# Kernel optimization log

Hardware: AMD Instinct MI355X
Metric: run time of the kernel (lower is better)

Reference implementation:

```python
import jax, jax.numpy as jnp
import numpy as np

B, N, D_H, D_K = 1024, 200, 512, 512
C_CLIP = 10.0  # tanh clipping constant C from out_attention default


def setup_inputs() -> dict:
    key = jax.random.key(0)
    k1, k2, k3, k4, k5 = jax.random.split(key, 5)
    d_c = 3 * D_H
    # xavier_uniform-ish scale (gain 1.414) approximated with scaled normals
    s_q = 1.414 * (2.0 / (d_c + D_K)) ** 0.5
    s_k = 1.414 * (2.0 / (D_H + D_K)) ** 0.5
    return {
        "n": N,
        "H": jax.random.normal(k1, (B, N, D_H), dtype=jnp.float32),
        "W_Q": jax.random.normal(k2, (d_c, D_K), dtype=jnp.float32) * s_q,
        "W_K": jax.random.normal(k3, (D_H, D_K), dtype=jnp.float32) * s_k,
        "v_1": jax.random.normal(k4, (D_H,), dtype=jnp.float32) * 0.1,
        "v_f": jax.random.normal(k5, (D_H,), dtype=jnp.float32) * 0.1,
    }


def reference(n, H, W_Q, W_K, v_1, v_f):
    Bsz, n_nodes, d_h = H.shape
    d_k = W_K.shape[1]
    inv_sqrt_dk = 1.0 / jnp.sqrt(jnp.asarray(d_k, H.dtype))

    H_bar = jnp.mean(H, axis=-2)  # (B, d_h)  == 1/n * sum over nodes
    K = H @ W_K                   # (B, n, d_k): W_K fixed across steps, hoist out of loop

    h_c0 = jnp.concatenate(
        [H_bar,
         jnp.broadcast_to(v_1, (Bsz, d_h)),
         jnp.broadcast_to(v_f, (Bsz, d_h))], axis=-1)  # (B, 3*d_h)

    keys = jax.random.split(jax.random.key(42), n)
    batch_ix = jnp.arange(Bsz)

    def step(carry, xs):
        h_c, H_pi_1 = carry           # (B, 3dh), (B, dh)
        i, k = xs
        Q = h_c @ W_Q                 # (B, d_k)
        U = jnp.einsum('bk,bnk->bn', Q, K) * inv_sqrt_dk  # (B, n)
        logits = C_CLIP * jnp.tanh(U)
        # multinomial(softmax(logits), 1) == categorical(logits)
        pi = jax.random.categorical(k, logits, axis=-1)   # (B,)
        H_pi = H[batch_ix, pi]        # (B, d_h) row gather
        H_pi_1 = jnp.where(i == 0, H_pi, H_pi_1)          # freeze first pick
        h_c_new = jnp.concatenate([H_bar, H_pi, H_pi_1], axis=-1)
        return (h_c_new, H_pi_1), pi

    init = (h_c0, jnp.zeros_like(H_bar))
    _, pis = jax.lax.scan(step, init, (jnp.arange(n), keys))  # pis: (n, B)
    # original duplicates step-0 sample: Pi = cat(Pi_0, Pi_0, Pi_1, ..., Pi_{n-1})
    Pi = jnp.concatenate([pis[:1], pis], axis=0).T  # (B, n+1)
    return Pi
```

## Files before the change

### kernel.cpp

```cpp
#include <hip/hip_runtime.h>
#include <math.h>

#define BSZ 1024
#define NNODE 200
#define DH 512
#define DK 512
#define NSTEP 200
#define G 2
#define TPB 512

typedef float f4 __attribute__((ext_vector_type(4)));

__device__ __forceinline__ unsigned rotl32(unsigned x, int r) {
  return (x << r) | (x >> (32 - r));
}

__device__ __forceinline__ void tf2x32(unsigned k0, unsigned k1,
                                       unsigned c0, unsigned c1,
                                       unsigned& o0, unsigned& o1) {
  unsigned ks2 = k0 ^ k1 ^ 0x1BD11BDAu;
  unsigned x0 = c0 + k0, x1 = c1 + k1;
#define TF_RND(r) { x0 += x1; x1 = rotl32(x1, (r)); x1 ^= x0; }
  TF_RND(13) TF_RND(15) TF_RND(26) TF_RND(6)
  x0 += k1;  x1 += ks2 + 1u;
  TF_RND(17) TF_RND(29) TF_RND(16) TF_RND(24)
  x0 += ks2; x1 += k0 + 2u;
  TF_RND(13) TF_RND(15) TF_RND(26) TF_RND(6)
  x0 += k0;  x1 += k1 + 3u;
  TF_RND(17) TF_RND(29) TF_RND(16) TF_RND(24)
  x0 += k1;  x1 += ks2 + 4u;
  TF_RND(13) TF_RND(15) TF_RND(26) TF_RND(6)
  x0 += ks2; x1 += k0 + 5u;
#undef TF_RND
  o0 = x0; o1 = x1;
}

__device__ __forceinline__ void step_key(int i, unsigned& k0, unsigned& k1) {
  tf2x32(0u, 42u, 0u, (unsigned)i, k0, k1);
}
__device__ __forceinline__ unsigned elem_bits(unsigned k0, unsigned k1, unsigned m) {
  unsigned o0, o1;
  tf2x32(k0, k1, 0u, m, o0, o1);
  return o0 ^ o1;
}

__device__ __forceinline__ float xla_tanh_f32(float x) {
  const float kMax = 7.90531110763549805f;
  float xc = fminf(fmaxf(x, -kMax), kMax);
  float x2 = xc * xc;
  float p = -2.76076847742355e-16f;
  p = __builtin_fmaf(x2, p, 2.00018790482477e-13f);
  p = __builtin_fmaf(x2, p, -8.60467152213735e-11f);
  p = __builtin_fmaf(x2, p, 5.12229709037114e-08f);
  p = __builtin_fmaf(x2, p, 1.48572235717979e-05f);
  p = __builtin_fmaf(x2, p, 6.37261928875436e-04f);
  p = __builtin_fmaf(x2, p, 4.89352455891786e-03f);
  float num = xc * p;
  float q = 1.19825839466702e-06f;
  q = __builtin_fmaf(x2, q, 1.18534705686654e-04f);
  q = __builtin_fmaf(x2, q, 2.26843463243900e-03f);
  q = __builtin_fmaf(x2, q, 4.89352518554385e-03f);
  float r = num / q;
  return (fabsf(x) < 0.0004f) ? x : r;
}

__device__ __forceinline__ float xla_log_f32(float x) {
#pragma clang fp contract(off)
  unsigned bits = __float_as_uint(x);
  int e = (int)((bits >> 23) & 0xffu) - 126;
  float m = __uint_as_float((bits & 0x007fffffu) | 0x3f000000u);
  bool c = m < 0.707106781186547524f;
  e = c ? (e - 1) : e;
  m = c ? (m + m) : m;
  m = m - 1.0f;
  float z = m * m;
  float y = 7.0376836292e-2f;
  y = y * m + (-1.1514610310e-1f);
  y = y * m + 1.1676998740e-1f;
  y = y * m + (-1.2420140846e-1f);
  y = y * m + 1.4249322787e-1f;
  y = y * m + (-1.6668057665e-1f);
  y = y * m + 2.0000714765e-1f;
  y = y * m + (-2.4999993993e-1f);
  y = y * m + 3.3333331174e-1f;
  y = y * m;
  y = y * z;
  float ef = (float)e;
  float t1 = ef * (-2.12194440e-4f);
  y = y + t1;
  float t2 = z * 0.5f;
  y = y - t2;
  float r = m + y;
  float t3 = ef * 0.693359375f;
  r = r + t3;
  return r;
}

template<bool NT>
__device__ __forceinline__ float u_dot(const f4* __restrict__ Kb4,
                                       const float* __restrict__ qrow) {
  float l[16];
#pragma unroll
  for (int j = 0; j < 16; j++) l[j] = 0.0f;
#pragma unroll 1
  for (int g = 0; g < 8; g++) {
    f4 kv[16];
#pragma unroll
    for (int m = 0; m < 16; m++) {
      const f4* p = &Kb4[(size_t)(g * 16 + m) * NNODE];
      kv[m] = NT ? __builtin_nontemporal_load(p) : *p;
    }
    {
#pragma clang fp contract(off)
#pragma unroll
      for (int m = 0; m < 16; m++) {
        const int r = (4 * m) & 15;
        float p0 = kv[m][0] * qrow[g * 64 + 4 * m + 0];
        l[r + 0] = l[r + 0] + p0;
        float p1 = kv[m][1] * qrow[g * 64 + 4 * m + 1];
        l[r + 1] = l[r + 1] + p1;
        float p2 = kv[m][2] * qrow[g * 64 + 4 * m + 2];
        l[r + 2] = l[r + 2] + p2;
        float p3 = kv[m][3] * qrow[g * 64 + 4 * m + 3];
        l[r + 3] = l[r + 3] + p3;
      }
    }
  }
  {
#pragma clang fp contract(off)
#pragma unroll
    for (int j = 0; j < 8; j++) l[j] = l[j] + l[j + 8];
#pragma unroll
    for (int j = 0; j < 4; j++) l[j] = l[j] + l[j + 4];
#pragma unroll
    for (int j = 0; j < 2; j++) l[j] = l[j] + l[j + 2];
    return l[0] + l[1];
  }
}


__global__ void k_hbar(const float* __restrict__ H, float* __restrict__ Hbar) {
#pragma clang fp contract(off)
  int idx = blockIdx.x * 256 + threadIdx.x;
  int b = idx >> 9, d = idx & 511;
  const float* p = H + (size_t)b * NNODE * DH + d;
  float s = 0.0f;
  for (int n = 0; n < NNODE; n++) s = s + p[(size_t)n * DH];
  Hbar[idx] = s / 200.0f;
}

__global__ __launch_bounds__(256) void k_K(const float* __restrict__ H,
                                           const float* __restrict__ WK,
                                           float* __restrict__ KT) {
  __shared__ float hr[8][DH];
  __shared__ float ts[DK * 9];
  int g = blockIdx.x;
  int b = g / 25;
  int r0 = (g % 25) * 8;
  int t = threadIdx.x;
  const float* Hb = H + (size_t)b * NNODE * DH + (size_t)r0 * DH;
  for (int e = t; e < 8 * DH; e += 256) hr[e >> 9][e & 511] = Hb[e];
  __syncthreads();
  int k0 = t, k1 = t + 256;
  float a[8][2];
#pragma unroll
  for (int r = 0; r < 8; r++) { a[r][0] = 0.0f; a[r][1] = 0.0f; }
  for (int d = 0; d < DH; d++) {
    float w0 = WK[(size_t)d * DK + k0], w1 = WK[(size_t)d * DK + k1];
#pragma unroll
    for (int r = 0; r < 8; r++) {
      a[r][0] = __builtin_fmaf(hr[r][d], w0, a[r][0]);
      a[r][1] = __builtin_fmaf(hr[r][d], w1, a[r][1]);
    }
  }
#pragma unroll
  for (int r = 0; r < 8; r++) {
    ts[k0 * 9 + r] = a[r][0];
    ts[k1 * 9 + r] = a[r][1];
  }
  __syncthreads();
  float* Ko = KT + (size_t)b * DK * NNODE;
  for (int i = t; i < (DK / 4) * 8; i += 256) {
    int c = i >> 3, r = i & 7;
    float4 v = make_float4(ts[(4 * c + 0) * 9 + r], ts[(4 * c + 1) * 9 + r],
                           ts[(4 * c + 2) * 9 + r], ts[(4 * c + 3) * 9 + r]);
    *(float4*)(Ko + ((size_t)c * NNODE + (r0 + r)) * 4) = v;
  }
}

__global__ __launch_bounds__(256) void k_acc512(const float* __restrict__ Hbar,
                                                const float* __restrict__ WQ,
                                                float* __restrict__ acc) {
  __shared__ float hb[DH];
  int b = blockIdx.x, t = threadIdx.x;
  for (int e = t; e < DH; e += 256) hb[e] = Hbar[(size_t)b * DH + e];
  __syncthreads();
  int j0 = t, j1 = t + 256;
  float a0 = 0.0f, a1 = 0.0f;
  for (int k = 0; k < DH; k++) {
    float w0 = WQ[(size_t)k * DK + j0], w1 = WQ[(size_t)k * DK + j1];
    a0 = __builtin_fmaf(hb[k], w0, a0);
    a1 = __builtin_fmaf(hb[k], w1, a1);
  }
  acc[(size_t)b * DK + j0] = a0;
  acc[(size_t)b * DK + j1] = a1;
}

__global__ __launch_bounds__(TPB, 4) void k_mega(const float* __restrict__ KT,
                                                 const float* __restrict__ acc,
                                                 const float* __restrict__ WQ,
                                                 const float* __restrict__ H,
                                                 const float* __restrict__ v1,
                                                 const float* __restrict__ vf,
                                                 int* __restrict__ out) {
  __shared__ float hpI[DH][G];
  __shared__ float hp0I[DH][G];
  __shared__ float Qs[G][DK];
  __shared__ float accs[G][DK];
  __shared__ float zl[G][NNODE];
  int t = threadIdx.x;
  int b0 = blockIdx.x * G;
  int bb = t >> 8;
  int tl = t & 255;
  int b = b0 + bb;
  const bool useNT = (blockIdx.x & 1) != 0;
  const f4* Kb4 = (const f4*)(KT + (size_t)b * DK * NNODE) + tl;
  const float* qrow = &Qs[bb][0];

  for (int e = t; e < G * DK; e += TPB) {
    int b2 = e >> 9, j = e & 511;
    accs[b2][j] = acc[(size_t)(b0 + b2) * DK + j];
  }
  for (int e = t; e < DH; e += TPB) {
    float a = v1[e], bv = vf[e];
#pragma unroll
    for (int b2 = 0; b2 < G; b2++) { hpI[e][b2] = a; hp0I[e][b2] = bv; }
  }
  __syncthreads();

  for (int step = 0; step < NSTEP; step++) {
    {
      float a0 = accs[0][t], a1 = accs[1][t];
      const float* Wp = WQ + (size_t)512 * DK + t;
      for (int k = 0; k < DH; k += 4) {
        float w0 = Wp[(size_t)(k + 0) * DK];
        float w1 = Wp[(size_t)(k + 1) * DK];
        float w2 = Wp[(size_t)(k + 2) * DK];
        float w3 = Wp[(size_t)(k + 3) * DK];
        float2 h0 = *(const float2*)&hpI[k + 0][0];
        float2 h1 = *(const float2*)&hpI[k + 1][0];
        float2 h2 = *(const float2*)&hpI[k + 2][0];
        float2 h3 = *(const float2*)&hpI[k + 3][0];
        a0 = __builtin_fmaf(h0.x, w0, a0); a1 = __builtin_fmaf(h0.y, w0, a1);
        a0 = __builtin_fmaf(h1.x, w1, a0); a1 = __builtin_fmaf(h1.y, w1, a1);
        a0 = __builtin_fmaf(h2.x, w2, a0); a1 = __builtin_fmaf(h2.y, w2, a1);
        a0 = __builtin_fmaf(h3.x, w3, a0); a1 = __builtin_fmaf(h3.y, w3, a1);
      }
      const float* Wp2 = WQ + (size_t)1024 * DK + t;
      for (int k = 0; k < DH; k += 4) {
        float w0 = Wp2[(size_t)(k + 0) * DK];
        float w1 = Wp2[(size_t)(k + 1) * DK];
        float w2 = Wp2[(size_t)(k + 2) * DK];
        float w3 = Wp2[(size_t)(k + 3) * DK];
        float2 h0 = *(const float2*)&hp0I[k + 0][0];
        float2 h1 = *(const float2*)&hp0I[k + 1][0];
        float2 h2 = *(const float2*)&hp0I[k + 2][0];
        float2 h3 = *(const float2*)&hp0I[k + 3][0];
        a0 = __builtin_fmaf(h0.x, w0, a0); a1 = __builtin_fmaf(h0.y, w0, a1);
        a0 = __builtin_fmaf(h1.x, w1, a0); a1 = __builtin_fmaf(h1.y, w1, a1);
        a0 = __builtin_fmaf(h2.x, w2, a0); a1 = __builtin_fmaf(h2.y, w2, a1);
        a0 = __builtin_fmaf(h3.x, w3, a0); a1 = __builtin_fmaf(h3.y, w3, a1);
      }
      Qs[0][t] = a0; Qs[1][t] = a1;
    }
    __syncthreads();

    if (tl < NNODE) {
      float U = useNT ? u_dot<true>(Kb4, qrow) : u_dot<false>(Kb4, qrow);
      {
#pragma clang fp contract(off)
        const float inv = 1.0f / sqrtf(512.0f);
        float u = U * inv;
        float logit = 10.0f * xla_tanh_f32(u);
        unsigned kk0, kk1;
        step_key(step, kk0, kk1);
        unsigned bits = elem_bits(kk0, kk1, (unsigned)(b * NNODE + tl));
        unsigned fb = (bits >> 9) | 0x3F800000u;
        float uf = __uint_as_float(fb) - 1.0f;
        const float tinyf = 1.17549435e-38f;
        float v = uf * 1.0f;
        v = v + tinyf;
        v = fmaxf(tinyf, v);
        float L1 = xla_log_f32(v);
        float gmb = -xla_log_f32(-L1);
        zl[bb][tl] = gmb + logit;
      }
    }
    __syncthreads();

    int pi;
    {
      float bv = -__builtin_inff();
      int bi = 0;
      for (int n = (tl & 63); n < NNODE; n += 64) {
        float zv = zl[bb][n];
        if (zv > bv) { bv = zv; bi = n; }
      }
      for (int off = 32; off; off >>= 1) {
        float ov = __shfl_down(bv, off);
        int   oi = __shfl_down(bi, off);
        if (ov > bv || (ov == bv && oi < bi)) { bv = ov; bi = oi; }
      }
      pi = __shfl(bi, 0);
    }
    if (tl == 0) {
      out[b * (NSTEP + 1) + step + 1] = pi;
      if (step == 0) out[b * (NSTEP + 1)] = pi;
    }
    {
      const float* src = H + ((size_t)b * NNODE + pi) * DH;
      for (int e = tl; e < DH; e += 256) hpI[e][bb] = src[e];
    }
    __syncthreads();
    if (step == 0) {
      for (int e = t; e < DH * G; e += TPB) hp0I[e >> 1][e & 1] = hpI[e >> 1][e & 1];
      __syncthreads();
    }
  }
}

extern "C" void kernel_launch(void* const* d_in, const int* in_sizes, int n_in,
                              void* d_out, int out_size, void* d_ws, size_t ws_size,
                              hipStream_t stream) {
  (void)in_sizes; (void)n_in; (void)out_size; (void)ws_size;
  const float* H  = (const float*)d_in[1];
  const float* WQ = (const float*)d_in[2];
  const float* WK = (const float*)d_in[3];
  const float* v1 = (const float*)d_in[4];
  const float* vf = (const float*)d_in[5];
  int* out = (int*)d_out;

  float* ws = (float*)d_ws;
  const size_t KSZ = (size_t)BSZ * NNODE * DK;
  const size_t S = (size_t)BSZ * 512;
  float* KT   = ws;
  float* Hbar = ws + KSZ;
  float* acc  = ws + KSZ + S;

  k_hbar  <<<2048, 256, 0, stream>>>(H, Hbar);
  k_K     <<<BSZ * 25, 256, 0, stream>>>(H, WK, KT);
  k_acc512<<<BSZ, 256, 0, stream>>>(Hbar, WQ, acc);
  k_mega  <<<BSZ / G, TPB, 0, stream>>>(KT, acc, WQ, H, v1, vf, out);
}
```

Measured before the change: 19.82 ms.

## Cache first K chunk in LDS and double-buffer K loads in u_dot

The first 8 f4 rows (32 of 512 k-dims) of each batch's transposed K are kept in shared memory once per block, so each step reads that slice from LDS instead of global memory. The remaining 15 chunks are streamed through two register buffers, so the load of one chunk overlaps the compute of the previous one. This is meant to cut per-step global K traffic and hide load latency. It adds about 51KB of LDS per block, which may reduce occupancy under launch_bounds(512,4), and may raise register pressure.

```diff
diff --git a/kernel.cpp b/kernel.cpp
--- a/kernel.cpp
+++ b/kernel.cpp
@@ -8,6 +8,7 @@
 #define NSTEP 200
 #define G 2
 #define TPB 512
+#define CCACHE 8
 
 typedef float f4 __attribute__((ext_vector_type(4)));
 
@@ -96,34 +97,55 @@
   return r;
 }
 
+__device__ __forceinline__ void load8(f4 (&buf)[8], const f4* __restrict__ Kb4,
+                                      int h, bool nt) {
+#pragma unroll
+  for (int m = 0; m < 8; m++) {
+    const f4* p = &Kb4[(size_t)(h * 8 + m) * NNODE];
+    buf[m] = nt ? __builtin_nontemporal_load(p) : *p;
+  }
+}
+__device__ __forceinline__ void comp8(const f4 (&buf)[8], float (&l)[16],
+                                      const float* __restrict__ qrow, int h) {
+#pragma clang fp contract(off)
+#pragma unroll
+  for (int m = 0; m < 8; m++) {
+    const int r = (4 * m) & 15;
+    const int qb = (h * 8 + m) * 4;
+    float p0 = buf[m][0] * qrow[qb + 0];
+    l[r + 0] = l[r + 0] + p0;
+    float p1 = buf[m][1] * qrow[qb + 1];
+    l[r + 1] = l[r + 1] + p1;
+    float p2 = buf[m][2] * qrow[qb + 2];
+    l[r + 2] = l[r + 2] + p2;
+    float p3 = buf[m][3] * qrow[qb + 3];
+    l[r + 3] = l[r + 3] + p3;
+  }
+}
+
 template<bool NT>
 __device__ __forceinline__ float u_dot(const f4* __restrict__ Kb4,
-                                       const float* __restrict__ qrow) {
+                                       const float* __restrict__ qrow,
+                                       const f4* __restrict__ cKrow, int tl) {
   float l[16];
 #pragma unroll
   for (int j = 0; j < 16; j++) l[j] = 0.0f;
-#pragma unroll 1
-  for (int g = 0; g < 8; g++) {
-    f4 kv[16];
-#pragma unroll
-    for (int m = 0; m < 16; m++) {
-      const f4* p = &Kb4[(size_t)(g * 16 + m) * NNODE];
-      kv[m] = NT ? __builtin_nontemporal_load(p) : *p;
-    }
-    {
-#pragma clang fp contract(off)
-#pragma unroll
-      for (int m = 0; m < 16; m++) {
-        const int r = (4 * m) & 15;
-        float p0 = kv[m][0] * qrow[g * 64 + 4 * m + 0];
-        l[r + 0] = l[r + 0] + p0;
-        float p1 = kv[m][1] * qrow[g * 64 + 4 * m + 1];
-        l[r + 1] = l[r + 1] + p1;
-        float p2 = kv[m][2] * qrow[g * 64 + 4 * m + 2];
-        l[r + 2] = l[r + 2] + p2;
-        float p3 = kv[m][3] * qrow[g * 64 + 4 * m + 3];
-        l[r + 3] = l[r + 3] + p3;
-      }
+  f4 A[8], B[8];
+  load8(A, Kb4, 1, NT);
+  load8(B, Kb4, 2, NT);
+  {
+    f4 C[8];
+#pragma unroll
+    for (int m = 0; m < 8; m++) C[m] = cKrow[m * NNODE + tl];
+    comp8(C, l, qrow, 0);
+  }
+#pragma unroll
+  for (int h = 1; h <= 15; h += 2) {
+    comp8(A, l, qrow, h);
+    if (h + 2 <= 15) load8(A, Kb4, h + 2, NT);
+    if (h + 1 <= 15) {
+      comp8(B, l, qrow, h + 1);
+      if (h + 3 <= 15) load8(B, Kb4, h + 3, NT);
     }
   }
   {
@@ -218,6 +240,7 @@
   __shared__ float Qs[G][DK];
   __shared__ float accs[G][DK];
   __shared__ float zl[G][NNODE];
+  __shared__ f4 cacheK[G][CCACHE * NNODE];
   int t = threadIdx.x;
   int b0 = blockIdx.x * G;
   int bb = t >> 8;
@@ -226,6 +249,7 @@
   const bool useNT = (blockIdx.x & 1) != 0;
   const f4* Kb4 = (const f4*)(KT + (size_t)b * DK * NNODE) + tl;
   const float* qrow = &Qs[bb][0];
+  const f4* cKrow = &cacheK[bb][0];
 
   for (int e = t; e < G * DK; e += TPB) {
     int b2 = e >> 9, j = e & 511;
@@ -235,6 +259,12 @@
     float a = v1[e], bv = vf[e];
 #pragma unroll
     for (int b2 = 0; b2 < G; b2++) { hpI[e][b2] = a; hp0I[e][b2] = bv; }
+  }
+  for (int idx = t; idx < G * CCACHE * NNODE; idx += TPB) {
+    int b2 = idx / (CCACHE * NNODE);
+    int rem = idx - b2 * (CCACHE * NNODE);
+    cacheK[b2][rem] =
+        ((const f4*)KT)[(size_t)(b0 + b2) * (DK / 4) * NNODE + rem];
   }
   __syncthreads();
 
@@ -276,7 +306,8 @@
     __syncthreads();
 
     if (tl < NNODE) {
-      float U = useNT ? u_dot<true>(Kb4, qrow) : u_dot<false>(Kb4, qrow);
+      float U = useNT ? u_dot<true>(Kb4, qrow, cKrow, tl)
+                      : u_dot<false>(Kb4, qrow, cKrow, tl);
       {
 #pragma clang fp contract(off)
         const float inv = 1.0f / sqrtf(512.0f);
```

After: 78.74 ms. +297.2%, slower.
